# Kernel tuning notes

Measured on AMD Instinct MI355X. Metric: run time of the kernel, lower is better.

The kernel has to match this reference:

```python
import jax, jax.numpy as jnp
import numpy as np

D_MODEL = 1024
NUM_HEADS = 16
D_K = D_MODEL // NUM_HEADS
THETA = 10000.0


def _rope(x, pos):
    # x: [B, H, S, D_K], pos: [S]
    angles = 1.0 / (THETA ** (jnp.arange(0, D_K, 2, dtype=jnp.float32) / D_K))  # [D_K/2]
    ang = pos.astype(jnp.float32)[:, None] * angles  # [S, D_K/2]
    cos = jnp.repeat(jnp.cos(ang), 2, axis=-1)  # [S, D_K]
    sin = jnp.repeat(jnp.sin(ang), 2, axis=-1)
    x2 = x.reshape(*x.shape[:-1], D_K // 2, 2)
    xr = jnp.stack([-x2[..., 1], x2[..., 0]], axis=-1).reshape(x.shape)
    return x * cos + xr * sin


def setup_inputs() -> dict:
    key = jax.random.key(0)
    ks = jax.random.split(key, 5)
    B, S = 2, 2048
    sd = np.sqrt(2.0 / (D_MODEL + D_MODEL))
    return {
        "x": jax.random.normal(ks[0], (B, S, D_MODEL), dtype=jnp.float32),
        "token_positions": jnp.arange(S, dtype=jnp.int32),
        "Wq": jax.random.normal(ks[1], (D_MODEL, D_MODEL), dtype=jnp.float32) * sd,
        "Wk": jax.random.normal(ks[2], (D_MODEL, D_MODEL), dtype=jnp.float32) * sd,
        "Wv": jax.random.normal(ks[3], (D_MODEL, D_MODEL), dtype=jnp.float32) * sd,
        "Wo": jax.random.normal(ks[4], (D_MODEL, D_MODEL), dtype=jnp.float32) * sd,
    }


def reference(x, token_positions, Wq, Wk, Wv, Wo):
    B, S, _ = x.shape

    def proj_heads(W):
        y = jnp.einsum('bsd,ed->bse', x, W)  # weight stored [d_out, d_in]
        return y.reshape(B, S, NUM_HEADS, D_K).transpose(0, 2, 1, 3)  # [B,H,S,Dk]

    q = _rope(proj_heads(Wq), token_positions)
    k = _rope(proj_heads(Wk), token_positions)
    v = proj_heads(Wv)

    scores = jnp.einsum('bhqd,bhkd->bhqk', q, k) / np.sqrt(D_K)  # [B,H,S,S]
    causal = jnp.tril(jnp.ones((S, S), dtype=bool))
    scores = jnp.where(causal, scores, -jnp.inf)
    attn = jax.nn.softmax(scores, axis=-1)
    out = jnp.einsum('bhqk,bhkd->bhqd', attn, v)  # [B,H,S,Dk]
    out = out.transpose(0, 2, 1, 3).reshape(B, S, D_MODEL)
    return jnp.einsum('bsd,ed->bse', out, Wo)
```

## Files before the change

### kernel.cpp

```cpp
#include <hip/hip_runtime.h>
#include <hip/hip_bf16.h>
#include <cstdint>
#include <cmath>

#define SEQ 2048
#define NH 16
#define DM 1024
#define BATCH 2

typedef short bf16x8 __attribute__((ext_vector_type(8)));
typedef float f32x4 __attribute__((ext_vector_type(4)));
typedef const void __attribute__((address_space(1)))* gas_t;
typedef void __attribute__((address_space(3)))* las_t;

#if __has_builtin(__builtin_amdgcn_exp2f)
#define EXP2(x) __builtin_amdgcn_exp2f(x)
#else
#define EXP2(x) __expf((x) * 0.6931471805599453f)
#endif

#define QSCALE 0.18033688011112042f

static __device__ __forceinline__ unsigned short f2bf(float f) {
    union { __hip_bfloat16 h; unsigned short u; } cv;
    cv.h = __float2bfloat16(f);
    return cv.u;
}
static __device__ __forceinline__ float bf2f(unsigned short u) {
    union { unsigned short u; __hip_bfloat16 h; } cv;
    cv.u = u;
    return __bfloat162float(cv.h);
}

static __device__ __forceinline__ void gload_lds16(const void* g, void* l) {
    __builtin_amdgcn_global_load_lds(
        reinterpret_cast<gas_t>(reinterpret_cast<uintptr_t>(g)),
        reinterpret_cast<las_t>(reinterpret_cast<uintptr_t>(l)),
        16, 0, 0);
}

__global__ __launch_bounds__(256) void cvt_all(
    const float* __restrict__ x,  const float* __restrict__ wq,
    const float* __restrict__ wk, const float* __restrict__ wv,
    const float* __restrict__ wo,
    unsigned short* __restrict__ xb, unsigned short* __restrict__ wqkv,
    unsigned short* __restrict__ wob) {
    int blk = blockIdx.x;
    const float* src; unsigned short* dst; int base;
    if (blk < 4096)      { src = x;  dst = xb;              base = blk; }
    else if (blk < 5120) { src = wq; dst = wqkv;            base = blk - 4096; }
    else if (blk < 6144) { src = wk; dst = wqkv + 1048576;  base = blk - 5120; }
    else if (blk < 7168) { src = wv; dst = wqkv + 2097152;  base = blk - 6144; }
    else                 { src = wo; dst = wob;             base = blk - 7168; }
    int i = base * 256 + threadIdx.x;
    float4 v = reinterpret_cast<const float4*>(src)[i];
    ushort4 o;
    o.x = f2bf(v.x); o.y = f2bf(v.y); o.z = f2bf(v.z); o.w = f2bf(v.w);
    reinterpret_cast<ushort4*>(dst)[i] = o;
}

template<int OUT_BF16>
__global__ __launch_bounds__(256) void gemm_bt(
    const unsigned short* __restrict__ A,
    const unsigned short* __restrict__ B,
    void* __restrict__ C, int M, int N, int K) {
    __shared__ unsigned short As[128 * 32];
    __shared__ unsigned short Bs[128 * 32];
    const int tid = threadIdx.x;
    const int lane = tid & 63, wid = tid >> 6;
    const int wr = wid >> 1, wc = wid & 1;
    const int ln15 = lane & 15, kq = lane >> 4;
    const int bm = blockIdx.y, bn = blockIdx.x;

    f32x4 acc[4][4] = {};
    const int nk = K >> 5;
    for (int kt = 0; kt < nk; ++kt) {
        #pragma unroll
        for (int i = 0; i < 2; ++i) {
            int c = i * 256 + tid;
            int row = c >> 2, k8 = (c & 3) << 3;
            size_t gofsA = (size_t)(bm * 128 + row) * K + kt * 32 + k8;
            size_t gofsB = (size_t)(bn * 128 + row) * K + kt * 32 + k8;
            unsigned ldsoff = (unsigned)(i * 256 + wid * 64) * 16;
            gload_lds16(A + gofsA, (char*)As + ldsoff);
            gload_lds16(B + gofsB, (char*)Bs + ldsoff);
        }
        __syncthreads();
        bf16x8 af[4], bf[4];
        #pragma unroll
        for (int m = 0; m < 4; ++m)
            af[m] = *reinterpret_cast<const bf16x8*>(&As[(wr * 64 + m * 16 + ln15) * 32 + kq * 8]);
        #pragma unroll
        for (int n = 0; n < 4; ++n)
            bf[n] = *reinterpret_cast<const bf16x8*>(&Bs[(wc * 64 + n * 16 + ln15) * 32 + kq * 8]);
        #pragma unroll
        for (int m = 0; m < 4; ++m)
            #pragma unroll
            for (int n = 0; n < 4; ++n)
                acc[m][n] = __builtin_amdgcn_mfma_f32_16x16x32_bf16(af[m], bf[n], acc[m][n], 0, 0, 0);
        __syncthreads();
    }
    #pragma unroll
    for (int m = 0; m < 4; ++m) {
        #pragma unroll
        for (int n = 0; n < 4; ++n) {
            int col = bn * 128 + wc * 64 + n * 16 + ln15;
            #pragma unroll
            for (int j = 0; j < 4; ++j) {
                int row = bm * 128 + wr * 64 + m * 16 + kq * 4 + j;
                if constexpr (OUT_BF16 != 0)
                    ((unsigned short*)C)[(size_t)row * N + col] = f2bf(acc[m][n][j]);
                else
                    ((float*)C)[(size_t)row * N + col] = acc[m][n][j];
            }
        }
    }
}

__global__ __launch_bounds__(512) void gemm256_bt(
    const unsigned short* __restrict__ A,
    const unsigned short* __restrict__ B,
    unsigned short* __restrict__ Qh, unsigned short* __restrict__ Kh,
    unsigned short* __restrict__ Vtr, const float2* __restrict__ tab, int K) {
    __shared__ unsigned short As[2][256 * 64];
    __shared__ unsigned short Bs[2][256 * 64];
    const int tid = threadIdx.x;
    const int lane = tid & 63, wid = tid >> 6;
    const int wm = wid >> 2, wn = wid & 3;
    const int ln15 = lane & 15, g = lane >> 4;
    const int bm = blockIdx.y, bn = blockIdx.x;

    const unsigned short* aSrc[4];
    const unsigned short* bSrc[4];
    #pragma unroll
    for (int p = 0; p < 4; ++p) {
        int c = tid + (p << 9);
        int row = c >> 3, slot = c & 7;
        aSrc[p] = A + (size_t)(bm * 256 + row) * K + ((slot ^ (row & 7)) << 3);
        bSrc[p] = B + (size_t)(bn * 256 + row) * K + ((slot ^ (row & 7)) << 3);
    }
    auto stageA = [&](int kt, int h) {
        #pragma unroll
        for (int p = 2 * h; p < 2 * h + 2; ++p) {
            unsigned dst = (unsigned)(tid + (p << 9)) << 4;
            gload_lds16(aSrc[p] + kt * 64, (char*)As[kt & 1] + dst);
        }
    };
    auto stageB = [&](int kt, int h) {
        #pragma unroll
        for (int p = 2 * h; p < 2 * h + 2; ++p) {
            unsigned dst = (unsigned)(tid + (p << 9)) << 4;
            gload_lds16(bSrc[p] + kt * 64, (char*)Bs[kt & 1] + dst);
        }
    };

    const unsigned ps0 = (unsigned)((g ^ (ln15 & 7)) << 4);
    const unsigned ps1 = (unsigned)(((4 + g) ^ (ln15 & 7)) << 4);
    const unsigned aBase = (unsigned)(wm * 128 + ln15) * 128;
    const unsigned bBase = (unsigned)(wn * 64 + ln15) * 128;

    f32x4 acc[8][4] = {};
    const int nkt = K >> 6;
    const int nit = nkt >> 1;

    stageA(0, 0); stageA(0, 1);
    stageB(0, 0); stageB(0, 1);
    stageB(1, 0); stageB(1, 1);
    asm volatile("s_waitcnt vmcnt(0)" ::: "memory");
    __builtin_amdgcn_s_barrier();

    for (int j = 0; j < nit; ++j) {
        const int t0 = 2 * j, t1 = 2 * j + 1;
        const bool more = (t0 + 2) < nkt;
        #pragma unroll
        for (int grp = 0; grp < 2; ++grp) {
            const char* Ab = (const char*)As[grp];
            const char* Bb = (const char*)Bs[grp];
            bf16x8 bfr[4][2];
            #pragma unroll
            for (int q = 0; q < 4; ++q) {
                if (q == 0) {
                    #pragma unroll
                    for (int nf = 0; nf < 4; ++nf) {
                        bfr[nf][0] = *reinterpret_cast<const bf16x8*>(Bb + bBase + nf * 2048 + ps0);
                        bfr[nf][1] = *reinterpret_cast<const bf16x8*>(Bb + bBase + nf * 2048 + ps1);
                    }
                }
                bf16x8 af0 = *reinterpret_cast<const bf16x8*>(Ab + aBase + (2 * q) * 2048 + ps0);
                bf16x8 af1 = *reinterpret_cast<const bf16x8*>(Ab + aBase + (2 * q) * 2048 + ps1);
                bf16x8 af2 = *reinterpret_cast<const bf16x8*>(Ab + aBase + (2 * q + 1) * 2048 + ps0);
                bf16x8 af3 = *reinterpret_cast<const bf16x8*>(Ab + aBase + (2 * q + 1) * 2048 + ps1);

                if (grp == 0) {
                    if (q == 0) stageA(t1, 0);
                    else if (q == 1) stageA(t1, 1);
                    else if (q == 2) { if (more) stageB(t0 + 2, 0); }
                    else {
                        if (more) { stageB(t0 + 2, 1);
                                    asm volatile("s_waitcnt vmcnt(4)" ::: "memory"); }
                        else      { asm volatile("s_waitcnt vmcnt(0)" ::: "memory"); }
                    }
                } else {
                    if (q == 0)      { if (more) stageA(t0 + 2, 0); }
                    else if (q == 1) { if (more) stageA(t0 + 2, 1); }
                    else if (q == 2) { if (more) stageB(t1 + 2, 0); }
                    else {
                        if (more) { stageB(t1 + 2, 1);
                                    asm volatile("s_waitcnt vmcnt(4)" ::: "memory"); }
                        else      { asm volatile("s_waitcnt vmcnt(0)" ::: "memory"); }
                    }
                }

                __builtin_amdgcn_s_barrier();
                asm volatile("s_waitcnt lgkmcnt(0)" ::: "memory");
                __builtin_amdgcn_s_setprio(1);
                #pragma unroll
                for (int nf = 0; nf < 4; ++nf) {
                    acc[2 * q][nf] = __builtin_amdgcn_mfma_f32_16x16x32_bf16(af0, bfr[nf][0], acc[2 * q][nf], 0, 0, 0);
                    acc[2 * q][nf] = __builtin_amdgcn_mfma_f32_16x16x32_bf16(af1, bfr[nf][1], acc[2 * q][nf], 0, 0, 0);
                    acc[2 * q + 1][nf] = __builtin_amdgcn_mfma_f32_16x16x32_bf16(af2, bfr[nf][0], acc[2 * q + 1][nf], 0, 0, 0);
                    acc[2 * q + 1][nf] = __builtin_amdgcn_mfma_f32_16x16x32_bf16(af3, bfr[nf][1], acc[2 * q + 1][nf], 0, 0, 0);
                }
                __builtin_amdgcn_s_setprio(0);
                __builtin_amdgcn_s_barrier();
            }
        }
    }

    const int sel = bn >> 2;
    const int colBase = (bn & 3) * 256 + wn * 64;
    #pragma unroll
    for (int mf = 0; mf < 8; ++mf) {
        int row0 = bm * 256 + wm * 128 + mf * 16 + g * 4;
        int b = row0 >> 11, s0 = row0 & 2047;
        #pragma unroll
        for (int nf = 0; nf < 4; ++nf) {
            int col = colBase + nf * 16 + ln15;
            int h = col >> 6, d = col & 63;
            if (sel == 2) {
                ushort4 w;
                w.x = f2bf(acc[mf][nf][0]); w.y = f2bf(acc[mf][nf][1]);
                w.z = f2bf(acc[mf][nf][2]); w.w = f2bf(acc[mf][nf][3]);
                *reinterpret_cast<ushort4*>(
                    &Vtr[(((size_t)(b * NH + h)) * 64 + d) * SEQ + s0]) = w;
            } else {
                unsigned short* dst = (sel == 0) ? Qh : Kh;
                const float sc = (sel == 0) ? QSCALE : 1.f;
                int i = d >> 1;
                #pragma unroll
                for (int j2 = 0; j2 < 4; ++j2) {
                    float v = acc[mf][nf][j2];
                    float p = __shfl_xor(v, 1);
                    float2 cs = tab[((s0 + j2) << 5) + i];
                    float o = (d & 1) ? (v * cs.x + p * cs.y)
                                      : (v * cs.x - p * cs.y);
                    dst[(((size_t)(b * NH + h)) * SEQ + (s0 + j2)) * 64 + d] =
                        f2bf(o * sc);
                }
            }
        }
    }
}

__global__ __launch_bounds__(256) void rope_table(const int* __restrict__ pos,
                                                  float2* __restrict__ tab) {
    int idx = blockIdx.x * 256 + threadIdx.x;
    int s = idx >> 5, i = idx & 31;
    float fpos = (float)pos[s];
    float freq = exp2f(-(float)i * (13.287712379549449f / 32.0f));
    float ang = fpos * freq, sn, cs;
    sincosf(ang, &sn, &cs);
    tab[idx] = make_float2(cs, sn);
}

__global__ __launch_bounds__(128) void attn_kernel(
    const unsigned short* __restrict__ Qh, const unsigned short* __restrict__ Kh,
    const unsigned short* __restrict__ Vt, unsigned short* __restrict__ Out) {
    __shared__ unsigned short Kb[2][64 * 64];
    __shared__ unsigned short Vb[2][64 * 64];
    __shared__ unsigned short Plds[2][16 * 72];

    const int tid = threadIdx.x;
    const int wid = tid >> 6, lane = tid & 63;
    const int ln15 = lane & 15, g = lane >> 4;
    const int bid = blockIdx.x;
    const int bh = bid & 31;
    const int pb = bid >> 5;

    const unsigned short* Qp = Qh + (size_t)bh * SEQ * 64;
    const unsigned short* Kp = Kh + (size_t)bh * SEQ * 64;
    const unsigned short* Vp = Vt + (size_t)bh * 64 * SEQ;
    char* Pc = (char*)Plds[wid];

    const unsigned short* kSrc[4];
    const unsigned short* vSrc[4];
    #pragma unroll
    for (int p = 0; p < 4; ++p) {
        int c = tid + (p << 7);
        int row = c >> 3, slot = c & 7;
        kSrc[p] = Kp + (size_t)row * 64 + ((slot ^ (row & 7)) << 3);
        vSrc[p] = Vp + (size_t)row * SEQ + ((slot ^ (row & 7)) << 3);
    }

    auto stage = [&](int kb, int buf) {
        #pragma unroll
        for (int p = 0; p < 4; ++p) {
            unsigned bb = (unsigned)(wid * 1024 + p * 2048);
            gload_lds16(kSrc[p] + (size_t)kb * 64, (char*)Kb[buf] + bb);
            gload_lds16(vSrc[p] + kb, (char*)Vb[buf] + bb);
        }
    };

    unsigned kOff[4][2], vOff[4][2];
    #pragma unroll
    for (int s = 0; s < 4; ++s) {
        int r = ln15 + 16 * s;
        kOff[s][0] = r * 128 + ((g ^ (r & 7)) << 4);
        kOff[s][1] = r * 128 + (((4 + g) ^ (r & 7)) << 4);
    }
    #pragma unroll
    for (int c = 0; c < 4; ++c) {
        int d = c * 16 + ln15;
        vOff[c][0] = d * 128 + ((g ^ (d & 7)) << 4);
        vOff[c][1] = d * 128 + (((4 + g) ^ (d & 7)) << 4);
    }
    const unsigned pW = (unsigned)(ln15 * 144 + 8 * g);
    const unsigned pR = (unsigned)(ln15 * 144 + 16 * g);

    const int b = bh >> 4, h = bh & 15;

    for (int bi = 0; bi < 2; ++bi) {
        const int bnd = bi ? (63 - pb) : pb;
        const int qb = bnd * 32 + wid * 16;
        const int nt = (bnd + 2) >> 1;
        const int thr = qb + ln15 - 4 * g;

        bf16x8 aq0 = *reinterpret_cast<const bf16x8*>(Qp + (size_t)(qb + ln15) * 64 + g * 8);
        bf16x8 aq1 = *reinterpret_cast<const bf16x8*>(Qp + (size_t)(qb + ln15) * 64 + 32 + g * 8);

        f32x4 oacc[4] = {};
        float lsum = 0.f;

        stage(0, 0);

        for (int t = 0; t < nt; ++t) {
            const int kb = t << 6;
            const int cur = t & 1;
            if (t + 1 < nt) {
                stage((t + 1) << 6, cur ^ 1);
                asm volatile("s_waitcnt vmcnt(8)" ::: "memory");
            } else {
                asm volatile("s_waitcnt vmcnt(0)" ::: "memory");
            }
            __builtin_amdgcn_s_barrier();

            const char* K0 = (const char*)Kb[cur];
            const char* V0 = (const char*)Vb[cur];
            bf16x8 kf[8], bv[8];
            #pragma unroll
            for (int s = 0; s < 4; ++s) {
                kf[2 * s]     = *reinterpret_cast<const bf16x8*>(K0 + kOff[s][0]);
                kf[2 * s + 1] = *reinterpret_cast<const bf16x8*>(K0 + kOff[s][1]);
            }
            #pragma unroll
            for (int c = 0; c < 4; ++c) {
                bv[2 * c]     = *reinterpret_cast<const bf16x8*>(V0 + vOff[c][0]);
                bv[2 * c + 1] = *reinterpret_cast<const bf16x8*>(V0 + vOff[c][1]);
            }

            const f32x4 z = {};
            f32x4 sq[4];
            #pragma unroll
            for (int s = 0; s < 4; ++s) {
                sq[s] = __builtin_amdgcn_mfma_f32_16x16x32_bf16(kf[2 * s], aq0, z, 0, 0, 0);
                sq[s] = __builtin_amdgcn_mfma_f32_16x16x32_bf16(kf[2 * s + 1], aq1, sq[s], 0, 0, 0);
            }

            float pv[4][4];
            if (t == nt - 1) {
                #pragma unroll
                for (int s = 0; s < 4; ++s)
                    #pragma unroll
                    for (int j = 0; j < 4; ++j)
                        pv[s][j] = (j <= thr - kb - 16 * s) ? EXP2(sq[s][j]) : 0.f;
            } else {
                #pragma unroll
                for (int s = 0; s < 4; ++s)
                    #pragma unroll
                    for (int j = 0; j < 4; ++j)
                        pv[s][j] = EXP2(sq[s][j]);
            }
            #pragma unroll
            for (int s = 0; s < 4; ++s)
                lsum += (pv[s][0] + pv[s][1]) + (pv[s][2] + pv[s][3]);

            #pragma unroll
            for (int s = 0; s < 4; ++s) {
                ushort4 w;
                w.x = f2bf(pv[s][0]); w.y = f2bf(pv[s][1]);
                w.z = f2bf(pv[s][2]); w.w = f2bf(pv[s][3]);
                *reinterpret_cast<ushort4*>(Pc + pW + 32 * s) = w;
            }
            asm volatile("s_waitcnt lgkmcnt(0)" ::: "memory");
            bf16x8 ap0 = *reinterpret_cast<const bf16x8*>(Pc + pR);
            bf16x8 ap1 = *reinterpret_cast<const bf16x8*>(Pc + pR + 64);
            #pragma unroll
            for (int c = 0; c < 4; ++c) {
                oacc[c] = __builtin_amdgcn_mfma_f32_16x16x32_bf16(ap0, bv[2 * c], oacc[c], 0, 0, 0);
                oacc[c] = __builtin_amdgcn_mfma_f32_16x16x32_bf16(ap1, bv[2 * c + 1], oacc[c], 0, 0, 0);
            }
            asm volatile("s_waitcnt lgkmcnt(0)" ::: "memory");
            __builtin_amdgcn_s_barrier();
        }

        float r = lsum;
        r += __shfl_xor(r, 16);
        r += __shfl_xor(r, 32);
        float linv = 1.f / r;
        float invj[4];
        #pragma unroll
        for (int j = 0; j < 4; ++j)
            invj[j] = __shfl(linv, 20 * g + j);
        #pragma unroll
        for (int c = 0; c < 4; ++c)
            #pragma unroll
            for (int j = 0; j < 4; ++j) {
                int s = qb + g * 4 + j;
                Out[((size_t)(b * SEQ + s)) * DM + h * 64 + c * 16 + ln15] =
                    f2bf(oacc[c][j] * invj[j]);
            }
    }
}

extern "C" void kernel_launch(void* const* d_in, const int* in_sizes, int n_in,
                              void* d_out, int out_size, void* d_ws, size_t ws_size,
                              hipStream_t stream) {
    const float* x = (const float*)d_in[0];
    const int* pos = (const int*)d_in[1];
    const float* Wq = (const float*)d_in[2];
    const float* Wk = (const float*)d_in[3];
    const float* Wv = (const float*)d_in[4];
    const float* Wo = (const float*)d_in[5];
    float* out = (float*)d_out;

    char* ws = (char*)d_ws;
    const size_t MB = 1024 * 1024;
    unsigned short* xb   = (unsigned short*)(ws + 0 * MB);
    unsigned short* wqkv = (unsigned short*)(ws + 8 * MB);
    unsigned short* wob  = (unsigned short*)(ws + 14 * MB);
    float2*         tab  = (float2*)       (ws + 40 * MB);
    unsigned short* qh   = (unsigned short*)(ws + 41 * MB);
    unsigned short* kh   = (unsigned short*)(ws + 49 * MB);
    unsigned short* vtr  = (unsigned short*)(ws + 57 * MB);
    unsigned short* att  = (unsigned short*)(ws + 65 * MB);

    cvt_all<<<8192, 256, 0, stream>>>(x, Wq, Wk, Wv, Wo, xb, wqkv, wob);
    rope_table<<<256, 256, 0, stream>>>(pos, tab);

    gemm256_bt<<<dim3(12, 16), 512, 0, stream>>>(xb, wqkv, qh, kh, vtr, tab, 1024);

    attn_kernel<<<1024, 128, 0, stream>>>(qh, kh, vtr, att);

    gemm_bt<0><<<dim3(8, 32), 256, 0, stream>>>(att, wob, out, 4096, 1024, 1024);
}
```

Measured before the change: 119.8 us.

## Retile QKV GEMM to 256x192 tiles with XCD-aware block mapping

Changes the fused QKV projection GEMM from 256x256 tiles on a 12x16 grid (192 blocks) to 256x192 tiles on 256 blocks, so every CU on the device gets a block. Block IDs are remapped so that each XCD handles a compact 4x8 group of tiles, aiming for better L2 reuse of A and B panels. The B staging and wait counts are adjusted for three loads per stage. The RoPE epilogue now has even lanes write packed pairs instead of each lane storing one scalar. The tradeoff is a smaller N tile per wave, which lowers MFMA work per LDS read of A.

```diff
diff --git a/kernel.cpp b/kernel.cpp
--- a/kernel.cpp
+++ b/kernel.cpp
@@ -123,21 +123,29 @@
     unsigned short* __restrict__ Qh, unsigned short* __restrict__ Kh,
     unsigned short* __restrict__ Vtr, const float2* __restrict__ tab, int K) {
     __shared__ unsigned short As[2][256 * 64];
-    __shared__ unsigned short Bs[2][256 * 64];
+    __shared__ unsigned short Bs[2][192 * 64];
     const int tid = threadIdx.x;
     const int lane = tid & 63, wid = tid >> 6;
     const int wm = wid >> 2, wn = wid & 3;
     const int ln15 = lane & 15, g = lane >> 4;
-    const int bm = blockIdx.y, bn = blockIdx.x;
+    const int bid = blockIdx.x;
+    const int xcd = bid & 7, lid = bid >> 3;
+    const int bm = (xcd >> 1) * 4 + (lid & 3);
+    const int bn = (xcd & 1) * 8 + (lid >> 2);
 
     const unsigned short* aSrc[4];
-    const unsigned short* bSrc[4];
     #pragma unroll
     for (int p = 0; p < 4; ++p) {
         int c = tid + (p << 9);
         int row = c >> 3, slot = c & 7;
         aSrc[p] = A + (size_t)(bm * 256 + row) * K + ((slot ^ (row & 7)) << 3);
-        bSrc[p] = B + (size_t)(bn * 256 + row) * K + ((slot ^ (row & 7)) << 3);
+    }
+    const unsigned short* bSrc[3];
+    #pragma unroll
+    for (int u = 0; u < 3; ++u) {
+        int c = tid + (u << 9);
+        int row = c >> 3, slot = c & 7;
+        bSrc[u] = B + (size_t)(bn * 192 + row) * K + ((slot ^ (row & 7)) << 3);
     }
     auto stageA = [&](int kt, int h) {
         #pragma unroll
@@ -146,27 +154,24 @@
             gload_lds16(aSrc[p] + kt * 64, (char*)As[kt & 1] + dst);
         }
     };
-    auto stageB = [&](int kt, int h) {
-        #pragma unroll
-        for (int p = 2 * h; p < 2 * h + 2; ++p) {
-            unsigned dst = (unsigned)(tid + (p << 9)) << 4;
-            gload_lds16(bSrc[p] + kt * 64, (char*)Bs[kt & 1] + dst);
-        }
+    auto stageB1 = [&](int kt, int u) {
+        unsigned dst = (unsigned)(tid + (u << 9)) << 4;
+        gload_lds16(bSrc[u] + kt * 64, (char*)Bs[kt & 1] + dst);
     };
 
     const unsigned ps0 = (unsigned)((g ^ (ln15 & 7)) << 4);
     const unsigned ps1 = (unsigned)(((4 + g) ^ (ln15 & 7)) << 4);
     const unsigned aBase = (unsigned)(wm * 128 + ln15) * 128;
-    const unsigned bBase = (unsigned)(wn * 64 + ln15) * 128;
-
-    f32x4 acc[8][4] = {};
+    const unsigned bBase = (unsigned)(wn * 48 + ln15) * 128;
+
+    f32x4 acc[8][3] = {};
     const int nkt = K >> 6;
     const int nit = nkt >> 1;
 
     stageA(0, 0); stageA(0, 1);
-    stageB(0, 0); stageB(0, 1);
-    stageB(1, 0); stageB(1, 1);
-    asm volatile("s_waitcnt vmcnt(0)" ::: "memory");
+    stageB1(0, 0); stageB1(0, 1); stageB1(0, 2);
+    stageB1(1, 0); stageB1(1, 1); stageB1(1, 2);
+    asm volatile("s_waitcnt vmcnt(3)" ::: "memory");
     __builtin_amdgcn_s_barrier();
 
     for (int j = 0; j < nit; ++j) {
@@ -176,12 +181,12 @@
         for (int grp = 0; grp < 2; ++grp) {
             const char* Ab = (const char*)As[grp];
             const char* Bb = (const char*)Bs[grp];
-            bf16x8 bfr[4][2];
+            bf16x8 bfr[3][2];
             #pragma unroll
             for (int q = 0; q < 4; ++q) {
                 if (q == 0) {
                     #pragma unroll
-                    for (int nf = 0; nf < 4; ++nf) {
+                    for (int nf = 0; nf < 3; ++nf) {
                         bfr[nf][0] = *reinterpret_cast<const bf16x8*>(Bb + bBase + nf * 2048 + ps0);
                         bfr[nf][1] = *reinterpret_cast<const bf16x8*>(Bb + bBase + nf * 2048 + ps1);
                     }
@@ -194,19 +199,19 @@
                 if (grp == 0) {
                     if (q == 0) stageA(t1, 0);
                     else if (q == 1) stageA(t1, 1);
-                    else if (q == 2) { if (more) stageB(t0 + 2, 0); }
+                    else if (q == 2) { if (more) { stageB1(t0 + 2, 0); stageB1(t0 + 2, 1); } }
                     else {
-                        if (more) { stageB(t0 + 2, 1);
-                                    asm volatile("s_waitcnt vmcnt(4)" ::: "memory"); }
+                        if (more) { stageB1(t0 + 2, 2);
+                                    asm volatile("s_waitcnt vmcnt(3)" ::: "memory"); }
                         else      { asm volatile("s_waitcnt vmcnt(0)" ::: "memory"); }
                     }
                 } else {
                     if (q == 0)      { if (more) stageA(t0 + 2, 0); }
                     else if (q == 1) { if (more) stageA(t0 + 2, 1); }
-                    else if (q == 2) { if (more) stageB(t1 + 2, 0); }
+                    else if (q == 2) { if (more) { stageB1(t1 + 2, 0); stageB1(t1 + 2, 1); } }
                     else {
-                        if (more) { stageB(t1 + 2, 1);
-                                    asm volatile("s_waitcnt vmcnt(4)" ::: "memory"); }
+                        if (more) { stageB1(t1 + 2, 2);
+                                    asm volatile("s_waitcnt vmcnt(3)" ::: "memory"); }
                         else      { asm volatile("s_waitcnt vmcnt(0)" ::: "memory"); }
                     }
                 }
@@ -215,7 +220,7 @@
                 asm volatile("s_waitcnt lgkmcnt(0)" ::: "memory");
                 __builtin_amdgcn_s_setprio(1);
                 #pragma unroll
-                for (int nf = 0; nf < 4; ++nf) {
+                for (int nf = 0; nf < 3; ++nf) {
                     acc[2 * q][nf] = __builtin_amdgcn_mfma_f32_16x16x32_bf16(af0, bfr[nf][0], acc[2 * q][nf], 0, 0, 0);
                     acc[2 * q][nf] = __builtin_amdgcn_mfma_f32_16x16x32_bf16(af1, bfr[nf][1], acc[2 * q][nf], 0, 0, 0);
                     acc[2 * q + 1][nf] = __builtin_amdgcn_mfma_f32_16x16x32_bf16(af2, bfr[nf][0], acc[2 * q + 1][nf], 0, 0, 0);
@@ -227,16 +232,17 @@
         }
     }
 
-    const int sel = bn >> 2;
-    const int colBase = (bn & 3) * 256 + wn * 64;
     #pragma unroll
     for (int mf = 0; mf < 8; ++mf) {
         int row0 = bm * 256 + wm * 128 + mf * 16 + g * 4;
         int b = row0 >> 11, s0 = row0 & 2047;
         #pragma unroll
-        for (int nf = 0; nf < 4; ++nf) {
-            int col = colBase + nf * 16 + ln15;
-            int h = col >> 6, d = col & 63;
+        for (int nf = 0; nf < 3; ++nf) {
+            int scol = bn * 192 + wn * 48 + nf * 16;
+            int sel = scol >> 10;
+            int c10 = scol & 1023;
+            int h = c10 >> 6;
+            int d = (c10 & 63) + ln15;
             if (sel == 2) {
                 ushort4 w;
                 w.x = f2bf(acc[mf][nf][0]); w.y = f2bf(acc[mf][nf][1]);
@@ -252,10 +258,14 @@
                     float v = acc[mf][nf][j2];
                     float p = __shfl_xor(v, 1);
                     float2 cs = tab[((s0 + j2) << 5) + i];
-                    float o = (d & 1) ? (v * cs.x + p * cs.y)
-                                      : (v * cs.x - p * cs.y);
-                    dst[(((size_t)(b * NH + h)) * SEQ + (s0 + j2)) * 64 + d] =
-                        f2bf(o * sc);
+                    float oe = v * cs.x - p * cs.y;
+                    float oo = p * cs.x + v * cs.y;
+                    if (!(d & 1)) {
+                        ushort2 w2;
+                        w2.x = f2bf(oe * sc); w2.y = f2bf(oo * sc);
+                        *reinterpret_cast<ushort2*>(
+                            &dst[(((size_t)(b * NH + h)) * SEQ + (s0 + j2)) * 64 + d]) = w2;
+                    }
                 }
             }
         }
@@ -457,7 +467,7 @@
     cvt_all<<<8192, 256, 0, stream>>>(x, Wq, Wk, Wv, Wo, xb, wqkv, wob);
     rope_table<<<256, 256, 0, stream>>>(pos, tab);
 
-    gemm256_bt<<<dim3(12, 16), 512, 0, stream>>>(xb, wqkv, qh, kh, vtr, tab, 1024);
+    gemm256_bt<<<256, 512, 0, stream>>>(xb, wqkv, qh, kh, vtr, tab, 1024);
 
     attn_kernel<<<1024, 128, 0, stream>>>(qh, kh, vtr, att);
 
```

After: 125.3 us. 1.05x slower.
